# Kernel tuning notes

Measured on AMD Instinct MI355X. Metric: run time of the kernel, lower is better.

Reference implementation:

```python
import jax, jax.numpy as jnp
import numpy as np

EMBED_DIMS = 1024
NUM_HEADS = 16
HEAD_DIMS = EMBED_DIMS // NUM_HEADS


def setup_inputs() -> dict:
    key = jax.random.key(0)
    k_x, k_wqkv, k_bqkv, k_wp, k_bp = jax.random.split(key, 5)
    B, N, D = 2, 2048, EMBED_DIMS
    x = jax.random.normal(k_x, (B, N, D), dtype=jnp.float32)
    # torch nn.Linear(in, out): weight [out, in], y = x @ W.T + b
    s = 1.0 / np.sqrt(D)
    W_qkv = jax.random.uniform(k_wqkv, (3 * D, D), jnp.float32, -s, s)
    b_qkv = jax.random.uniform(k_bqkv, (3 * D,), jnp.float32, -s, s)
    W_proj = jax.random.uniform(k_wp, (D, D), jnp.float32, -s, s)
    b_proj = jax.random.uniform(k_bp, (D,), jnp.float32, -s, s)
    return {"x": x, "W_qkv": W_qkv, "b_qkv": b_qkv, "W_proj": W_proj, "b_proj": b_proj}


def reference(x, W_qkv, b_qkv, W_proj, b_proj):
    B, N, D = x.shape
    H, Hd = NUM_HEADS, HEAD_DIMS
    # qkv projection: [B, N, 3, H, Hd] -> split q, k, v as [B, H, N, Hd]
    qkv = (x @ W_qkv.T + b_qkv).reshape(B, N, 3, H, Hd).transpose(2, 0, 3, 1, 4)
    q, k, v = qkv[0], qkv[1], qkv[2]
    scale = 1.0 / jnp.sqrt(jnp.asarray(Hd, x.dtype))
    attn = jnp.einsum("bhqd,bhkd->bhqk", q, k) * scale  # [B, H, N, N]
    attn = jax.nn.softmax(attn, axis=-1)
    out = jnp.einsum("bhqk,bhkd->bhqd", attn, v)  # [B, H, N, Hd]
    out = out.transpose(0, 2, 1, 3).reshape(B, N, D)
    out = out @ W_proj.T + b_proj
    return out
```

## Files before the change

kernel.cpp:

```cpp
#include <hip/hip_runtime.h>

typedef _Float16 f16x8 __attribute__((ext_vector_type(8)));
typedef __attribute__((ext_vector_type(4))) float f32x4;

static __device__ __forceinline__ unsigned short f2h(float f) {
  return __builtin_bit_cast(unsigned short, (_Float16)f);
}

static __device__ __forceinline__ unsigned int pk2(float a, float b) {
  return (unsigned int)f2h(a) | ((unsigned int)f2h(b) << 16);
}

#if __has_builtin(__builtin_amdgcn_exp2f)
#define EXP2(x) __builtin_amdgcn_exp2f(x)
#else
#define EXP2(x) exp2f(x)
#endif

#define GLOAD_LDS16(gp, lp)                                          \
  __builtin_amdgcn_global_load_lds(                                  \
      (const __attribute__((address_space(1))) unsigned int*)(gp),   \
      (__attribute__((address_space(3))) unsigned int*)(lp), 16, 0, 0)

__global__ __launch_bounds__(256) void cvt_all(
    const float* __restrict__ X, const float* __restrict__ Wq,
    const float* __restrict__ Wp, unsigned short* __restrict__ Xb,
    unsigned short* __restrict__ Wqb, unsigned short* __restrict__ Wpb) {
  const int i = blockIdx.x * 256 + threadIdx.x;
  const float4* src;
  unsigned short* dst;
  int off;
  if (i < 1048576) {
    src = (const float4*)X; dst = Xb; off = i;
  } else if (i < 1835008) {
    src = (const float4*)Wq; dst = Wqb; off = i - 1048576;
  } else {
    src = (const float4*)Wp; dst = Wpb; off = i - 1835008;
  }
  const float4 v = src[off];
  *(ushort4*)(dst + (size_t)off * 4) =
      make_ushort4(f2h(v.x), f2h(v.y), f2h(v.z), f2h(v.w));
}

__global__ __launch_bounds__(256, 3) void qkv_gemm(
    const unsigned short* __restrict__ Xb, const unsigned short* __restrict__ Wb,
    const float* __restrict__ bias, unsigned short* __restrict__ Qb,
    unsigned short* __restrict__ Kb, unsigned short* __restrict__ Vt) {
  __shared__ __align__(16) unsigned short A_sh[2][128 * 32];
  __shared__ __align__(16) unsigned short B_sh[2][128 * 32];
  const int n0 = blockIdx.x * 128, m0 = blockIdx.y * 128;
  const int tid = threadIdx.x, lane = tid & 63, wave = tid >> 6;
  const int wr = wave >> 1, wc = wave & 1;
  const int lm = lane & 15, lg = lane >> 4;
  const int r4 = lane >> 2;
  const int sg8 = (((lane & 3) ^ ((r4 >> 1) & 3)) * 8);
  const int lgx = (lg ^ ((lm >> 1) & 3)) * 8;

  f32x4 acc[4][4] = {};

#define QSTAGE(k0_, b_)                                                       \
  do {                                                                        \
    _Pragma("unroll")                                                         \
    for (int j = 0; j < 2; ++j) {                                             \
      const int chunk = wave * 2 + j;                                         \
      const int row = chunk * 16 + r4;                                        \
      GLOAD_LDS16(Xb + (size_t)(m0 + row) * 1024 + (k0_) + sg8,               \
                  &A_sh[b_][chunk * 512]);                                    \
      GLOAD_LDS16(Wb + (size_t)(n0 + row) * 1024 + (k0_) + sg8,               \
                  &B_sh[b_][chunk * 512]);                                    \
    }                                                                         \
  } while (0)

  QSTAGE(0, 0);

  for (int it = 0; it < 32; ++it) {
    const int cur = it & 1;
    __syncthreads();
    if (it < 31) QSTAGE((it + 1) * 32, cur ^ 1);

    f16x8 af[4], bfr[4];
#pragma unroll
    for (int mi = 0; mi < 4; ++mi)
      af[mi] = *(const f16x8*)&A_sh[cur][(wr * 64 + mi * 16 + lm) * 32 + lgx];
#pragma unroll
    for (int ni = 0; ni < 4; ++ni)
      bfr[ni] = *(const f16x8*)&B_sh[cur][(wc * 64 + ni * 16 + lm) * 32 + lgx];
    __builtin_amdgcn_s_setprio(1);
#pragma unroll
    for (int mi = 0; mi < 4; ++mi)
#pragma unroll
      for (int ni = 0; ni < 4; ++ni)
        acc[mi][ni] = __builtin_amdgcn_mfma_f32_16x16x32_f16(
            af[mi], bfr[ni], acc[mi][ni], 0, 0, 0);
    __builtin_amdgcn_s_setprio(0);
  }
#undef QSTAGE

  const float qscale = 0.18033688011112042f;
#pragma unroll
  for (int mi = 0; mi < 4; ++mi) {
#pragma unroll
    for (int ni = 0; ni < 4; ++ni) {
      const int gn = n0 + wc * 64 + ni * 16 + lm;
      const float bv = bias[gn];
      const int which = gn >> 10;
      const int h = (gn >> 6) & 15;
      const int hd = gn & 63;
      float v[4];
#pragma unroll
      for (int r = 0; r < 4; ++r) v[r] = acc[mi][ni][r] + bv;
      const int gm0 = m0 + wr * 64 + mi * 16 + lg * 4;
      const int bb = gm0 >> 11;
      const int nq0 = gm0 & 2047;
      if (which == 0) {
        unsigned short* p = Qb + (((size_t)bb * 16 + h) * 2048 + nq0) * 64 + hd;
        p[0] = f2h(v[0] * qscale);   p[64] = f2h(v[1] * qscale);
        p[128] = f2h(v[2] * qscale); p[192] = f2h(v[3] * qscale);
      } else if (which == 1) {
        unsigned short* p = Kb + (((size_t)bb * 16 + h) * 2048 + nq0) * 64 + hd;
        p[0] = f2h(v[0]);   p[64] = f2h(v[1]);
        p[128] = f2h(v[2]); p[192] = f2h(v[3]);
      } else {
        *(ushort4*)(Vt + (((size_t)bb * 16 + h) * 64 + hd) * 2048 + nq0) =
            make_ushort4(f2h(v[0]), f2h(v[1]), f2h(v[2]), f2h(v[3]));
      }
    }
  }
}

__global__ __launch_bounds__(512, 4) void attn_kernel(
    const unsigned short* __restrict__ Qb, const unsigned short* __restrict__ Kb,
    const unsigned short* __restrict__ Vt, unsigned short* __restrict__ Ob) {
  __shared__ __align__(16) unsigned short K_sh[2][2][64 * 32];
  __shared__ __align__(16) unsigned short V_sh[2][2][64 * 32];
  __shared__ __align__(16) f32x4 Om[4][4][64];
  __shared__ float Ls2[4][64];
  const int bh = blockIdx.y, q0 = blockIdx.x * 128;
  const size_t base = (size_t)bh * (2048 * 64);
  const unsigned short* Qp = Qb + base;
  const unsigned short* Kp = Kb + base;
  const unsigned short* Vp = Vt + base;
  const int tid = threadIdx.x, lane = tid & 63, wave = tid >> 6;
  const int lm = lane & 15, lg = lane >> 4;
  const int r4 = lane >> 2;
  const int sg8 = (((lane & 3) ^ ((r4 >> 1) & 3)) * 8);
  const int lgx = (lg ^ ((lm >> 1) & 3)) * 8;

  const int qg = wave >> 1;
  const int khalf = wave & 1;

  f16x8 qf[2][2];
#pragma unroll
  for (int mi = 0; mi < 2; ++mi)
#pragma unroll
    for (int kc = 0; kc < 2; ++kc)
      qf[mi][kc] = *(const f16x8*)(Qp +
          (size_t)(q0 + qg * 32 + mi * 16 + lm) * 64 + kc * 32 + lg * 8);

  f32x4 o[2][4] = {};
  float lsum[2] = {0.0f, 0.0f};

  const bool isV = wave >= 4;
  const int plane = wave & 1;
  const int half = (wave >> 1) & 1;

#define STAGE(kt_, b_)                                                        \
  do {                                                                        \
    if (!isV) {                                                               \
      _Pragma("unroll")                                                       \
      for (int qv = 0; qv < 2; ++qv)                                          \
        GLOAD_LDS16(Kp + (size_t)((kt_) * 64 + half * 32 + qv * 16 + r4) * 64 \
                        + plane * 32 + sg8,                                   \
                    &K_sh[b_][plane][(half * 2 + qv) * 512]);                 \
    } else {                                                                  \
      _Pragma("unroll")                                                       \
      for (int qv = 0; qv < 2; ++qv)                                          \
        GLOAD_LDS16(Vp + (size_t)(half * 32 + qv * 16 + r4) * 2048 +          \
                        (kt_) * 64 + plane * 32 + sg8,                        \
                    &V_sh[b_][plane][(half * 2 + qv) * 512]);                 \
    }                                                                         \
  } while (0)

  STAGE(0, 0);

  for (int kt = 0; kt < 32; ++kt) {
    const int cur = kt & 1;
    __syncthreads();
    if (kt < 31) STAGE(kt + 1, cur ^ 1);

    f32x4 s[2][2] = {};
#pragma unroll
    for (int kc = 0; kc < 2; ++kc) {
#pragma unroll
      for (int ni = 0; ni < 2; ++ni) {
        const f16x8 kf = *(const f16x8*)
            &K_sh[cur][kc][(khalf * 32 + ni * 16 + lm) * 32 + lgx];
        s[0][ni] = __builtin_amdgcn_mfma_f32_16x16x32_f16(
            kf, qf[0][kc], s[0][ni], 0, 0, 0);
        s[1][ni] = __builtin_amdgcn_mfma_f32_16x16x32_f16(
            kf, qf[1][kc], s[1][ni], 0, 0, 0);
      }
    }

    unsigned int Wp_[2][2][2];
#pragma unroll
    for (int mi = 0; mi < 2; ++mi)
#pragma unroll
      for (int ni = 0; ni < 2; ++ni) {
        const float p0 = EXP2(s[mi][ni][0]), p1 = EXP2(s[mi][ni][1]);
        const float p2 = EXP2(s[mi][ni][2]), p3 = EXP2(s[mi][ni][3]);
        lsum[mi] += (p0 + p1) + (p2 + p3);
        Wp_[mi][ni][0] = pk2(p0, p1);
        Wp_[mi][ni][1] = pk2(p2, p3);
      }

    f16x8 vb[4];
#pragma unroll
    for (int ni = 0; ni < 4; ++ni)
      vb[ni] = *(const f16x8*)&V_sh[cur][khalf][(ni * 16 + lm) * 32 + lgx];

#pragma unroll
    for (int mi = 0; mi < 2; ++mi) {
      auto t0 = __builtin_amdgcn_permlane32_swap(Wp_[mi][0][0], Wp_[mi][1][0],
                                                 false, false);
      auto u0 = __builtin_amdgcn_permlane16_swap(t0[0], t0[1], false, false);
      auto t1 = __builtin_amdgcn_permlane32_swap(Wp_[mi][0][1], Wp_[mi][1][1],
                                                 false, false);
      auto u1 = __builtin_amdgcn_permlane16_swap(t1[0], t1[1], false, false);
      union { unsigned int u[4]; f16x8 v; } pa;
      pa.u[0] = u0[0];
      pa.u[1] = u1[0];
      pa.u[2] = u0[1];
      pa.u[3] = u1[1];
#pragma unroll
      for (int ni = 0; ni < 4; ++ni)
        o[mi][ni] = __builtin_amdgcn_mfma_f32_16x16x32_f16(
            pa.v, vb[ni], o[mi][ni], 0, 0, 0);
    }
  }
#undef STAGE

  const int b = bh >> 4, h = bh & 15;
#pragma unroll
  for (int mi = 0; mi < 2; ++mi) {
    __syncthreads();
    if (khalf == 1) {
#pragma unroll
      for (int ni = 0; ni < 4; ++ni) Om[qg][ni][lane] = o[mi][ni];
      Ls2[qg][lane] = lsum[mi];
    }
    __syncthreads();
    if (khalf == 0) {
#pragma unroll
      for (int ni = 0; ni < 4; ++ni) {
        const f32x4 t = Om[qg][ni][lane];
        o[mi][ni][0] += t[0]; o[mi][ni][1] += t[1];
        o[mi][ni][2] += t[2]; o[mi][ni][3] += t[3];
      }
      float total = lsum[mi] + Ls2[qg][lane];
      total += __shfl_xor(total, 16);
      total += __shfl_xor(total, 32);
#pragma unroll
      for (int r = 0; r < 4; ++r) {
        const float inv = 1.0f / __shfl(total, (lane & 48) | (lg * 4 + r));
        const int nq = q0 + qg * 32 + mi * 16 + lg * 4 + r;
        unsigned short* p = Ob + ((size_t)(b * 2048 + nq) * 16 + h) * 64 + lm;
        p[0] = f2h(o[mi][0][r] * inv);
        p[16] = f2h(o[mi][1][r] * inv);
        p[32] = f2h(o[mi][2][r] * inv);
        p[48] = f2h(o[mi][3][r] * inv);
      }
    }
  }
}

__global__ __launch_bounds__(256) void proj_gemm(
    const unsigned short* __restrict__ A, const unsigned short* __restrict__ Wb,
    const float* __restrict__ bias, float* __restrict__ Out) {
  __shared__ __align__(16) unsigned short A_sh[2][64 * 32];
  __shared__ __align__(16) unsigned short B_sh[2][128 * 32];
  const int n0 = blockIdx.x * 128, m0 = blockIdx.y * 64;
  const int tid = threadIdx.x, lane = tid & 63, wave = tid >> 6;
  const int wr = wave >> 1, wc = wave & 1, lm = lane & 15, lg = lane >> 4;
  const int r4 = lane >> 2;
  const int sg8 = (((lane & 3) ^ ((r4 >> 1) & 3)) * 8);
  const int lgx = (lg ^ ((lm >> 1) & 3)) * 8;

  f32x4 acc[2][4] = {};

#define PSTAGE(k0_, b_)                                                       \
  do {                                                                        \
    {                                                                         \
      const int row = wave * 16 + r4;                                         \
      GLOAD_LDS16(A + (size_t)(m0 + row) * 1024 + (k0_) + sg8,                \
                  &A_sh[b_][wave * 512]);                                     \
    }                                                                         \
    _Pragma("unroll")                                                         \
    for (int j = 0; j < 2; ++j) {                                             \
      const int chunk = wave * 2 + j;                                         \
      const int row = chunk * 16 + r4;                                        \
      GLOAD_LDS16(Wb + (size_t)(n0 + row) * 1024 + (k0_) + sg8,               \
                  &B_sh[b_][chunk * 512]);                                    \
    }                                                                         \
  } while (0)

  PSTAGE(0, 0);

  for (int it = 0; it < 32; ++it) {
    const int cur = it & 1;
    __syncthreads();
    if (it < 31) PSTAGE((it + 1) * 32, cur ^ 1);

    f16x8 af[2], bfr[4];
#pragma unroll
    for (int mi = 0; mi < 2; ++mi)
      af[mi] = *(const f16x8*)&A_sh[cur][(wr * 32 + mi * 16 + lm) * 32 + lgx];
#pragma unroll
    for (int ni = 0; ni < 4; ++ni)
      bfr[ni] = *(const f16x8*)&B_sh[cur][(wc * 64 + ni * 16 + lm) * 32 + lgx];
#pragma unroll
    for (int mi = 0; mi < 2; ++mi)
#pragma unroll
      for (int ni = 0; ni < 4; ++ni)
        acc[mi][ni] = __builtin_amdgcn_mfma_f32_16x16x32_f16(
            af[mi], bfr[ni], acc[mi][ni], 0, 0, 0);
  }
#undef PSTAGE

#pragma unroll
  for (int mi = 0; mi < 2; ++mi)
#pragma unroll
    for (int ni = 0; ni < 4; ++ni) {
      const int gn = n0 + wc * 64 + ni * 16 + lm;
      const float bv = bias[gn];
#pragma unroll
      for (int r = 0; r < 4; ++r) {
        const int gm = m0 + wr * 32 + mi * 16 + lg * 4 + r;
        Out[(size_t)gm * 1024 + gn] = acc[mi][ni][r] + bv;
      }
    }
}

extern "C" void kernel_launch(void* const* d_in, const int* in_sizes, int n_in,
                              void* d_out, int out_size, void* d_ws, size_t ws_size,
                              hipStream_t stream) {
  const float* x      = (const float*)d_in[0];
  const float* W_qkv  = (const float*)d_in[1];
  const float* b_qkv  = (const float*)d_in[2];
  const float* W_proj = (const float*)d_in[3];
  const float* b_proj = (const float*)d_in[4];
  float* out = (float*)d_out;

  unsigned short* Qb  = (unsigned short*)d_ws;
  unsigned short* Kb  = Qb + 4194304;
  unsigned short* Vt  = Kb + 4194304;
  unsigned short* Ao  = Vt + 4194304;
  unsigned short* Xb  = Ao + 4194304;
  unsigned short* Wqb = Xb + 4194304;
  unsigned short* Wpb = Wqb + 3145728;

  cvt_all<<<8192, 256, 0, stream>>>(x, W_qkv, W_proj, Xb, Wqb, Wpb);
  qkv_gemm<<<dim3(24, 32), 256, 0, stream>>>(Xb, Wqb, b_qkv, Qb, Kb, Vt);
  attn_kernel<<<dim3(16, 32), 512, 0, stream>>>(Qb, Kb, Vt, Ao);
  proj_gemm<<<dim3(8, 64), 256, 0, stream>>>(Ao, Wpb, b_proj, out);
}
```

Before: 186.2 us.

## Compute softmax row sums via MFMA with ones, use packed RTZ convert and setprio

Replaces the per-lane VALU accumulation of softmax denominators with an extra MFMA against a vector of ones, so the row sum comes out in the same layout as the output and the cross-lane shuffles at the end go away. Converts probabilities to fp16 with the packed round-toward-zero instruction instead of two separate conversions. Wraps MFMA groups in s_setprio to favour matrix issue across waves. In exchange it adds one MFMA per row block per tile, and the row sum is now taken from fp16-rounded probabilities rather than the fp32 values.

```diff
diff --git a/kernel.cpp b/kernel.cpp
--- a/kernel.cpp
+++ b/kernel.cpp
@@ -10,6 +10,14 @@
 static __device__ __forceinline__ unsigned int pk2(float a, float b) {
   return (unsigned int)f2h(a) | ((unsigned int)f2h(b) << 16);
 }
+
+#if __has_builtin(__builtin_amdgcn_cvt_pkrtz)
+static __device__ __forceinline__ unsigned int pkrtz(float a, float b) {
+  return __builtin_bit_cast(unsigned int, __builtin_amdgcn_cvt_pkrtz(a, b));
+}
+#else
+#define pkrtz pk2
+#endif
 
 #if __has_builtin(__builtin_amdgcn_exp2f)
 #define EXP2(x) __builtin_amdgcn_exp2f(x)
@@ -133,8 +141,7 @@
     const unsigned short* __restrict__ Vt, unsigned short* __restrict__ Ob) {
   __shared__ __align__(16) unsigned short K_sh[2][2][64 * 32];
   __shared__ __align__(16) unsigned short V_sh[2][2][64 * 32];
-  __shared__ __align__(16) f32x4 Om[4][4][64];
-  __shared__ float Ls2[4][64];
+  __shared__ __align__(16) f32x4 Om[4][5][64];
   const int bh = blockIdx.y, q0 = blockIdx.x * 128;
   const size_t base = (size_t)bh * (2048 * 64);
   const unsigned short* Qp = Qb + base;
@@ -149,6 +156,10 @@
   const int qg = wave >> 1;
   const int khalf = wave & 1;
 
+  f16x8 vones;
+#pragma unroll
+  for (int j = 0; j < 8; ++j) vones[j] = (_Float16)1.0f;
+
   f16x8 qf[2][2];
 #pragma unroll
   for (int mi = 0; mi < 2; ++mi)
@@ -158,7 +169,7 @@
           (size_t)(q0 + qg * 32 + mi * 16 + lm) * 64 + kc * 32 + lg * 8);
 
   f32x4 o[2][4] = {};
-  float lsum[2] = {0.0f, 0.0f};
+  f32x4 o_ones[2] = {};
 
   const bool isV = wave >= 4;
   const int plane = wave & 1;
@@ -195,10 +206,12 @@
       for (int ni = 0; ni < 2; ++ni) {
         const f16x8 kf = *(const f16x8*)
             &K_sh[cur][kc][(khalf * 32 + ni * 16 + lm) * 32 + lgx];
+        __builtin_amdgcn_s_setprio(1);
         s[0][ni] = __builtin_amdgcn_mfma_f32_16x16x32_f16(
             kf, qf[0][kc], s[0][ni], 0, 0, 0);
         s[1][ni] = __builtin_amdgcn_mfma_f32_16x16x32_f16(
             kf, qf[1][kc], s[1][ni], 0, 0, 0);
+        __builtin_amdgcn_s_setprio(0);
       }
     }
 
@@ -209,9 +222,8 @@
       for (int ni = 0; ni < 2; ++ni) {
         const float p0 = EXP2(s[mi][ni][0]), p1 = EXP2(s[mi][ni][1]);
         const float p2 = EXP2(s[mi][ni][2]), p3 = EXP2(s[mi][ni][3]);
-        lsum[mi] += (p0 + p1) + (p2 + p3);
-        Wp_[mi][ni][0] = pk2(p0, p1);
-        Wp_[mi][ni][1] = pk2(p2, p3);
+        Wp_[mi][ni][0] = pkrtz(p0, p1);
+        Wp_[mi][ni][1] = pkrtz(p2, p3);
       }
 
     f16x8 vb[4];
@@ -232,10 +244,14 @@
       pa.u[1] = u1[0];
       pa.u[2] = u0[1];
       pa.u[3] = u1[1];
+      __builtin_amdgcn_s_setprio(1);
 #pragma unroll
       for (int ni = 0; ni < 4; ++ni)
         o[mi][ni] = __builtin_amdgcn_mfma_f32_16x16x32_f16(
             pa.v, vb[ni], o[mi][ni], 0, 0, 0);
+      o_ones[mi] = __builtin_amdgcn_mfma_f32_16x16x32_f16(
+          pa.v, vones, o_ones[mi], 0, 0, 0);
+      __builtin_amdgcn_s_setprio(0);
     }
   }
 #undef STAGE
@@ -247,7 +263,7 @@
     if (khalf == 1) {
 #pragma unroll
       for (int ni = 0; ni < 4; ++ni) Om[qg][ni][lane] = o[mi][ni];
-      Ls2[qg][lane] = lsum[mi];
+      Om[qg][4][lane] = o_ones[mi];
     }
     __syncthreads();
     if (khalf == 0) {
@@ -257,12 +273,10 @@
         o[mi][ni][0] += t[0]; o[mi][ni][1] += t[1];
         o[mi][ni][2] += t[2]; o[mi][ni][3] += t[3];
       }
-      float total = lsum[mi] + Ls2[qg][lane];
-      total += __shfl_xor(total, 16);
-      total += __shfl_xor(total, 32);
+      const f32x4 t4 = Om[qg][4][lane];
 #pragma unroll
       for (int r = 0; r < 4; ++r) {
-        const float inv = 1.0f / __shfl(total, (lane & 48) | (lg * 4 + r));
+        const float inv = 1.0f / (o_ones[mi][r] + t4[r]);
         const int nq = q0 + qg * 32 + mi * 16 + lg * 4 + r;
         unsigned short* p = Ob + ((size_t)(b * 2048 + nq) * 16 + h) * 64 + lm;
         p[0] = f2h(o[mi][0][r] * inv);
```

Result: no change. 184.0 us (-1.2%).
